# Kernel optimization log

Measured on AMD Instinct MI355X. Metric: run time of the kernel, lower is better.

The kernel has to match this reference:

```python
import jax, jax.numpy as jnp
import numpy as np

N, D_IN, D_H, K, E = 100000, 128, 256, 16, 3200000


def setup_inputs() -> dict:
    key = jax.random.key(0)
    ks = jax.random.split(key, 6)
    x = jax.random.normal(ks[0], (N, D_IN), dtype=jnp.float32)
    edge_index = jax.random.randint(ks[1], (2, E), 0, N, dtype=jnp.int64)
    # Linear params (stored as [in, out] for x @ W + b)
    W1 = jax.random.normal(ks[2], (D_IN, D_H), dtype=jnp.float32) * 0.05
    b1 = jnp.zeros((D_H,), dtype=jnp.float32)
    W2 = jax.random.normal(ks[3], (D_H, K), dtype=jnp.float32) * 0.05
    b2 = jnp.zeros((K,), dtype=jnp.float32)
    return {"x": x, "edge_index": edge_index, "W1": W1, "b1": b1, "W2": W2, "b2": b2}


def reference(x, edge_index, W1, b1, W2, b2):
    # 2-layer MLP + row softmax -> soft cluster assignments C [N, K]
    h = jax.nn.relu(x @ W1 + b1)
    C = jax.nn.softmax(h @ W2 + b2, axis=1)
    # trace((C C^T)^T @ adj) == sum over edges (u,v) of C[u] . C[v]
    # (exact, incl. duplicate edges, since to_dense_adj scatter-adds 1 per edge)
    src, dst = edge_index[0], edge_index[1]
    edge_sum = jnp.sum(C[src] * C[dst])  # [E, K] gathered dot products, reduced
    num_edges = jnp.asarray(edge_index.shape[1], dtype=C.dtype)  # adj.sum()
    modularity_loss = -edge_sum / num_edges
    return (C, modularity_loss)
```

## Files before the change

### kernel.cpp

```cpp
#include <hip/hip_runtime.h>

#define N_NODES 100000
#define D_INF   128
#define D_HID   256
#define K_CL    16
#define N_TILES (N_NODES / 16)
#define N_EDGES 3200000
#define EDGE_BLOCKS (N_EDGES / 1024)

typedef __attribute__((ext_vector_type(8))) __bf16  bf16x8;
typedef __attribute__((ext_vector_type(8))) unsigned short u16x8;
typedef __attribute__((ext_vector_type(4))) float   f32x4;
typedef __attribute__((ext_vector_type(2))) float   f32x2;
typedef __attribute__((ext_vector_type(4))) unsigned int u32x4;

__device__ __forceinline__ unsigned short f2bf(float f) {
    unsigned int u = __builtin_bit_cast(unsigned int, f);
    u += 0x7fffu + ((u >> 16) & 1u);
    return (unsigned short)(u >> 16);
}

__global__ void prep_kernel(const float* __restrict__ W1,
                            const float* __restrict__ W2,
                            unsigned short* __restrict__ w1t,
                            unsigned short* __restrict__ w2t)
{
    const int i = blockIdx.x * 256 + threadIdx.x;
    if (i < D_INF * D_HID) {
        const int n = i >> 7, k = i & 127;
        w1t[i] = f2bf(W1[k * D_HID + n]);
    }
    if (i < D_HID * K_CL) {
        const int t = i >> 8, n = i & 255;
        w2t[i] = f2bf(W2[n * K_CL + t]);
    }
}

#define W1S 136
#define CHS 40

__global__ __launch_bounds__(256, 2) void mlp_kernel(
    const float* __restrict__ x, const unsigned short* __restrict__ W1T,
    const float* __restrict__ b1, const unsigned short* __restrict__ W2T,
    const float* __restrict__ b2, float* __restrict__ C,
    unsigned char* __restrict__ C8)
{
    __shared__ unsigned short w1s[256 * W1S];
    __shared__ unsigned short chbuf[4][2][16 * CHS];
    __shared__ float b1s[D_HID];

    const int tid  = threadIdx.x;
    const int wv   = tid >> 6;
    const int lane = tid & 63;
    const int c    = lane & 15;
    const int q    = lane >> 4;

    #pragma unroll
    for (int it = 0; it < 16; ++it) {
        const int idx = it * 256 + tid;
        const int row = idx >> 4, ch = idx & 15;
        const uint4 v = ((const uint4*)W1T)[idx];
        *(uint4*)&w1s[row * W1S + ch * 8] = v;
    }
    if (tid < D_HID) b1s[tid] = b1[tid];

    bf16x8 w2f[8];
    #pragma unroll
    for (int kc2 = 0; kc2 < 8; ++kc2)
        w2f[kc2] = *(const bf16x8*)(W2T + (size_t)c * D_HID + kc2 * 32 + q * 8);
    const float b2v = b2[c];
    __syncthreads();

    unsigned short* const chA = &chbuf[wv][0][0];
    unsigned short* const chB = &chbuf[wv][1][0];

    const int wid     = blockIdx.x * 4 + wv;
    const int wstride = gridDim.x * 4;

    float4 xraw[8];
    {
        const float* xr = x + (size_t)(wid * 16 + c) * D_INF + q * 8;
        #pragma unroll
        for (int j = 0; j < 8; ++j)
            xraw[j] = *(const float4*)(xr + (j >> 1) * 32 + (j & 1) * 4);
    }

    for (int tile = wid; tile < N_TILES; tile += wstride) {
        const int m0 = tile * 16;

        const int nxt = tile + wstride;
        float4 xnxt[8];
        if (nxt < N_TILES) {
            const float* xr = x + (size_t)(nxt * 16 + c) * D_INF + q * 8;
            #pragma unroll
            for (int j = 0; j < 8; ++j)
                xnxt[j] = *(const float4*)(xr + (j >> 1) * 32 + (j & 1) * 4);
        }

        bf16x8 afr[4];
        #pragma unroll
        for (int kc = 0; kc < 4; ++kc) {
            const float4 xa = xraw[kc * 2], xb = xraw[kc * 2 + 1];
            u16x8 af;
            af[0] = f2bf(xa.x); af[1] = f2bf(xa.y); af[2] = f2bf(xa.z); af[3] = f2bf(xa.w);
            af[4] = f2bf(xb.x); af[5] = f2bf(xb.y); af[6] = f2bf(xb.z); af[7] = f2bf(xb.w);
            afr[kc] = __builtin_bit_cast(bf16x8, af);
        }

        f32x4 acc2 = (f32x4){0.f, 0.f, 0.f, 0.f};
        #pragma unroll
        for (int kc2 = 0; kc2 < 8; ++kc2) {
            unsigned short* const cb = (kc2 & 1) ? chB : chA;
            #pragma unroll
            for (int half = 0; half < 2; ++half) {
                const int nt = kc2 * 2 + half;
                f32x4 a1 = (f32x4){0.f, 0.f, 0.f, 0.f};
                #pragma unroll
                for (int kc = 0; kc < 4; ++kc) {
                    const bf16x8 bf =
                        *(const bf16x8*)&w1s[(nt * 16 + c) * W1S + kc * 32 + q * 8];
                    a1 = __builtin_amdgcn_mfma_f32_16x16x32_bf16(afr[kc], bf, a1, 0, 0, 0);
                }
                const float bv = b1s[nt * 16 + c];
                #pragma unroll
                for (int r = 0; r < 4; ++r)
                    cb[(4 * q + r) * CHS + half * 16 + c] =
                        f2bf(fmaxf(a1[r] + bv, 0.f));
            }
            const bf16x8 a2 = *(const bf16x8*)&cb[c * CHS + q * 8];
            acc2 = __builtin_amdgcn_mfma_f32_16x16x32_bf16(a2, w2f[kc2], acc2, 0, 0, 0);
        }

        #pragma unroll
        for (int r = 0; r < 4; ++r) {
            const float l = acc2[r] + b2v;
            float mx = l;
            mx = fmaxf(mx, __shfl_xor(mx, 1));
            mx = fmaxf(mx, __shfl_xor(mx, 2));
            mx = fmaxf(mx, __shfl_xor(mx, 4));
            mx = fmaxf(mx, __shfl_xor(mx, 8));
            const float e = __expf(l - mx);
            float sm = e;
            sm += __shfl_xor(sm, 1);
            sm += __shfl_xor(sm, 2);
            sm += __shfl_xor(sm, 4);
            sm += __shfl_xor(sm, 8);
            const float p = e / sm;
            const size_t o = (size_t)(m0 + 4 * q + r) * K_CL + c;
            C[o]  = p;
            C8[o] = (unsigned char)
                (__builtin_amdgcn_cvt_pk_fp8_f32(p, p, 0, false) & 0xff);
        }

        if (nxt < N_TILES) {
            #pragma unroll
            for (int j = 0; j < 8; ++j) xraw[j] = xnxt[j];
        }
    }
}

__global__ __launch_bounds__(256, 5) void edge_kernel(
    const int* __restrict__ ei, const unsigned char* __restrict__ C8,
    float* __restrict__ partials)
{
    __shared__ float red[4];
    const int tid  = threadIdx.x;
    const int lane = tid & 63;
    const int wv   = tid >> 6;
    const int base = (blockIdx.x * 4 + wv) * 256;

    int u[4], v[4];
    #pragma unroll
    for (int j = 0; j < 4; ++j) {
        u[j] = ei[base + j * 64 + lane];
        v[j] = ei[N_EDGES + base + j * 64 + lane];
    }

    u32x4 A[4], B[4];
    #pragma unroll
    for (int j = 0; j < 4; ++j) {
        A[j] = *(const u32x4*)(C8 + (size_t)u[j] * 16);
        B[j] = *(const u32x4*)(C8 + (size_t)v[j] * 16);
    }

    float s0 = 0.f, s1 = 0.f, s2 = 0.f, s3 = 0.f;
    #pragma unroll
    for (int j = 0; j < 4; ++j) {
        float t = 0.f;
        #pragma unroll
        for (int d = 0; d < 4; ++d) {
            const f32x2 a0 = __builtin_amdgcn_cvt_pk_f32_fp8(A[j][d], false);
            const f32x2 a1 = __builtin_amdgcn_cvt_pk_f32_fp8(A[j][d], true);
            const f32x2 b0 = __builtin_amdgcn_cvt_pk_f32_fp8(B[j][d], false);
            const f32x2 b1 = __builtin_amdgcn_cvt_pk_f32_fp8(B[j][d], true);
            t = fmaf(a0[0], b0[0], t);
            t = fmaf(a0[1], b0[1], t);
            t = fmaf(a1[0], b1[0], t);
            t = fmaf(a1[1], b1[1], t);
        }
        if (j == 0) s0 = t; else if (j == 1) s1 = t;
        else if (j == 2) s2 = t; else s3 = t;
    }
    float s = (s0 + s1) + (s2 + s3);

    s += __shfl_xor(s, 1);
    s += __shfl_xor(s, 2);
    s += __shfl_xor(s, 4);
    s += __shfl_xor(s, 8);
    s += __shfl_xor(s, 16);
    s += __shfl_xor(s, 32);
    if (lane == 0) red[wv] = s;
    __syncthreads();
    if (tid == 0) partials[blockIdx.x] = red[0] + red[1] + red[2] + red[3];
}

__global__ __launch_bounds__(256) void finalize_kernel(
    const float* __restrict__ partials, float* __restrict__ out)
{
    __shared__ float red[4];
    const int tid = threadIdx.x;
    float s = 0.f;
    for (int i = tid; i < EDGE_BLOCKS; i += 256) s += partials[i];
    s += __shfl_xor(s, 1);
    s += __shfl_xor(s, 2);
    s += __shfl_xor(s, 4);
    s += __shfl_xor(s, 8);
    s += __shfl_xor(s, 16);
    s += __shfl_xor(s, 32);
    if ((tid & 63) == 0) red[tid >> 6] = s;
    __syncthreads();
    if (tid == 0)
        out[(size_t)N_NODES * K_CL] =
            -(red[0] + red[1] + red[2] + red[3]) / (float)N_EDGES;
}

extern "C" void kernel_launch(void* const* d_in, const int* in_sizes, int n_in,
                              void* d_out, int out_size, void* d_ws, size_t ws_size,
                              hipStream_t stream) {
    const float* x  = (const float*)d_in[0];
    const int*   ei = (const int*)  d_in[1];
    const float* W1 = (const float*)d_in[2];
    const float* b1 = (const float*)d_in[3];
    const float* W2 = (const float*)d_in[4];
    const float* b2 = (const float*)d_in[5];
    float* out = (float*)d_out;

    unsigned short* w1t      = (unsigned short*)d_ws;
    unsigned short* w2t      = (unsigned short*)((char*)d_ws + 65536);
    unsigned char*  C8       = (unsigned char*)((char*)d_ws + 73760);
    float*          partials = (float*)((char*)d_ws + 1673760);

    prep_kernel<<<128, 256, 0, stream>>>(W1, W2, w1t, w2t);
    mlp_kernel<<<512, 256, 0, stream>>>(x, w1t, b1, w2t, b2, out, C8);
    edge_kernel<<<EDGE_BLOCKS, 256, 0, stream>>>(ei, C8, partials);
    finalize_kernel<<<1, 256, 0, stream>>>(partials, out);
}
```

Baseline: 152.8 us.

## Fold weight prep into MLP kernel and finalize into edge kernel via ticket

Removes the separate prep kernel: each MLP block now converts and transposes W1 and W2 from fp32 to bf16 itself while loading them into shared memory and registers. Removes the finalize kernel: edge blocks publish their partial sums and take an atomic ticket, and the last block to arrive performs the final reduction. This cuts two kernel launches and their inter-kernel gaps. In exchange, every MLP block does a redundant strided fp32 weight read and conversion, and the edge path adds an atomic and a fence per block.

```diff
diff --git a/kernel.cpp b/kernel.cpp
--- a/kernel.cpp
+++ b/kernel.cpp
@@ -20,30 +20,14 @@
     return (unsigned short)(u >> 16);
 }
 
-__global__ void prep_kernel(const float* __restrict__ W1,
-                            const float* __restrict__ W2,
-                            unsigned short* __restrict__ w1t,
-                            unsigned short* __restrict__ w2t)
-{
-    const int i = blockIdx.x * 256 + threadIdx.x;
-    if (i < D_INF * D_HID) {
-        const int n = i >> 7, k = i & 127;
-        w1t[i] = f2bf(W1[k * D_HID + n]);
-    }
-    if (i < D_HID * K_CL) {
-        const int t = i >> 8, n = i & 255;
-        w2t[i] = f2bf(W2[n * K_CL + t]);
-    }
-}
-
 #define W1S 136
 #define CHS 40
 
 __global__ __launch_bounds__(256, 2) void mlp_kernel(
-    const float* __restrict__ x, const unsigned short* __restrict__ W1T,
-    const float* __restrict__ b1, const unsigned short* __restrict__ W2T,
+    const float* __restrict__ x, const float* __restrict__ W1,
+    const float* __restrict__ b1, const float* __restrict__ W2,
     const float* __restrict__ b2, float* __restrict__ C,
-    unsigned char* __restrict__ C8)
+    unsigned char* __restrict__ C8, unsigned int* __restrict__ ticket)
 {
     __shared__ unsigned short w1s[256 * W1S];
     __shared__ unsigned short chbuf[4][2][16 * CHS];
@@ -55,19 +39,27 @@
     const int c    = lane & 15;
     const int q    = lane >> 4;
 
-    #pragma unroll
-    for (int it = 0; it < 16; ++it) {
-        const int idx = it * 256 + tid;
-        const int row = idx >> 4, ch = idx & 15;
-        const uint4 v = ((const uint4*)W1T)[idx];
-        *(uint4*)&w1s[row * W1S + ch * 8] = v;
+    if (blockIdx.x == 0 && tid == 0)
+        __hip_atomic_store(ticket, 0u, __ATOMIC_RELAXED,
+                           __HIP_MEMORY_SCOPE_AGENT);
+
+    #pragma unroll 4
+    for (int k = 0; k < 128; k += 2) {
+        const unsigned int lo = f2bf(W1[k * D_HID + tid]);
+        const unsigned int hi = f2bf(W1[(k + 1) * D_HID + tid]);
+        *(unsigned int*)&w1s[tid * W1S + k] = lo | (hi << 16);
     }
     if (tid < D_HID) b1s[tid] = b1[tid];
 
     bf16x8 w2f[8];
     #pragma unroll
-    for (int kc2 = 0; kc2 < 8; ++kc2)
-        w2f[kc2] = *(const bf16x8*)(W2T + (size_t)c * D_HID + kc2 * 32 + q * 8);
+    for (int kc2 = 0; kc2 < 8; ++kc2) {
+        u16x8 t;
+        #pragma unroll
+        for (int j = 0; j < 8; ++j)
+            t[j] = f2bf(W2[(kc2 * 32 + q * 8 + j) * K_CL + c]);
+        w2f[kc2] = __builtin_bit_cast(bf16x8, t);
+    }
     const float b2v = b2[c];
     __syncthreads();
 
@@ -161,9 +153,11 @@
 
 __global__ __launch_bounds__(256, 5) void edge_kernel(
     const int* __restrict__ ei, const unsigned char* __restrict__ C8,
-    float* __restrict__ partials)
+    float* __restrict__ partials, unsigned int* __restrict__ ticket,
+    float* __restrict__ out)
 {
     __shared__ float red[4];
+    __shared__ unsigned int is_last;
     const int tid  = threadIdx.x;
     const int lane = tid & 63;
     const int wv   = tid >> 6;
@@ -211,27 +205,33 @@
     s += __shfl_xor(s, 32);
     if (lane == 0) red[wv] = s;
     __syncthreads();
-    if (tid == 0) partials[blockIdx.x] = red[0] + red[1] + red[2] + red[3];
-}
-
-__global__ __launch_bounds__(256) void finalize_kernel(
-    const float* __restrict__ partials, float* __restrict__ out)
-{
-    __shared__ float red[4];
-    const int tid = threadIdx.x;
-    float s = 0.f;
-    for (int i = tid; i < EDGE_BLOCKS; i += 256) s += partials[i];
-    s += __shfl_xor(s, 1);
-    s += __shfl_xor(s, 2);
-    s += __shfl_xor(s, 4);
-    s += __shfl_xor(s, 8);
-    s += __shfl_xor(s, 16);
-    s += __shfl_xor(s, 32);
-    if ((tid & 63) == 0) red[tid >> 6] = s;
+    if (tid == 0) {
+        const float bs = red[0] + red[1] + red[2] + red[3];
+        __hip_atomic_store(&partials[blockIdx.x], bs, __ATOMIC_RELAXED,
+                           __HIP_MEMORY_SCOPE_AGENT);
+        __threadfence();
+        const unsigned int old = atomicAdd(ticket, 1u);
+        is_last = (old == (unsigned int)(EDGE_BLOCKS - 1)) ? 1u : 0u;
+    }
     __syncthreads();
-    if (tid == 0)
-        out[(size_t)N_NODES * K_CL] =
-            -(red[0] + red[1] + red[2] + red[3]) / (float)N_EDGES;
+
+    if (is_last) {
+        float t = 0.f;
+        for (int i = tid; i < EDGE_BLOCKS; i += 256)
+            t += __hip_atomic_load(&partials[i], __ATOMIC_RELAXED,
+                                   __HIP_MEMORY_SCOPE_AGENT);
+        t += __shfl_xor(t, 1);
+        t += __shfl_xor(t, 2);
+        t += __shfl_xor(t, 4);
+        t += __shfl_xor(t, 8);
+        t += __shfl_xor(t, 16);
+        t += __shfl_xor(t, 32);
+        if (lane == 0) red[wv] = t;
+        __syncthreads();
+        if (tid == 0)
+            out[(size_t)N_NODES * K_CL] =
+                -(red[0] + red[1] + red[2] + red[3]) / (float)N_EDGES;
+    }
 }
 
 extern "C" void kernel_launch(void* const* d_in, const int* in_sizes, int n_in,
@@ -245,13 +245,10 @@
     const float* b2 = (const float*)d_in[5];
     float* out = (float*)d_out;
 
-    unsigned short* w1t      = (unsigned short*)d_ws;
-    unsigned short* w2t      = (unsigned short*)((char*)d_ws + 65536);
-    unsigned char*  C8       = (unsigned char*)((char*)d_ws + 73760);
-    float*          partials = (float*)((char*)d_ws + 1673760);
-
-    prep_kernel<<<128, 256, 0, stream>>>(W1, W2, w1t, w2t);
-    mlp_kernel<<<512, 256, 0, stream>>>(x, w1t, b1, w2t, b2, out, C8);
-    edge_kernel<<<EDGE_BLOCKS, 256, 0, stream>>>(ei, C8, partials);
-    finalize_kernel<<<1, 256, 0, stream>>>(partials, out);
-}
+    unsigned char* C8       = (unsigned char*)d_ws;
+    float*         partials = (float*)((char*)d_ws + 1600000);
+    unsigned int*  ticket   = (unsigned int*)((char*)d_ws + 1612500);
+
+    mlp_kernel<<<512, 256, 0, stream>>>(x, W1, b1, W2, b2, out, C8, ticket);
+    edge_kernel<<<EDGE_BLOCKS, 256, 0, stream>>>(ei, C8, partials, ticket, out);
+}
```

Result: slower. 227.2 us (+48.7%).

## Process two row tiles per wave and fold weight conversion into MLP kernel

Applied to the files above, without the earlier changes.

Removes the separate weight-prep kernel; each MLP block now converts and transposes W1/W2 from fp32 into bf16 LDS/registers directly. Each wave handles two 16-row tiles per iteration, reusing each W1 LDS fragment for two MFMAs and giving independent MFMA chains, with the next pair's x prefetched. This saves a launch and LDS reads per tile but adds redundant strided fp32 weight loads in every block and more register pressure.

```diff
diff --git a/kernel.cpp b/kernel.cpp
--- a/kernel.cpp
+++ b/kernel.cpp
@@ -4,7 +4,7 @@
 #define D_INF   128
 #define D_HID   256
 #define K_CL    16
-#define N_TILES (N_NODES / 16)
+#define N_PAIRS (N_NODES / 32)
 #define N_EDGES 3200000
 #define EDGE_BLOCKS (N_EDGES / 1024)
 
@@ -20,28 +20,12 @@
     return (unsigned short)(u >> 16);
 }
 
-__global__ void prep_kernel(const float* __restrict__ W1,
-                            const float* __restrict__ W2,
-                            unsigned short* __restrict__ w1t,
-                            unsigned short* __restrict__ w2t)
-{
-    const int i = blockIdx.x * 256 + threadIdx.x;
-    if (i < D_INF * D_HID) {
-        const int n = i >> 7, k = i & 127;
-        w1t[i] = f2bf(W1[k * D_HID + n]);
-    }
-    if (i < D_HID * K_CL) {
-        const int t = i >> 8, n = i & 255;
-        w2t[i] = f2bf(W2[n * K_CL + t]);
-    }
-}
-
 #define W1S 136
 #define CHS 40
 
 __global__ __launch_bounds__(256, 2) void mlp_kernel(
-    const float* __restrict__ x, const unsigned short* __restrict__ W1T,
-    const float* __restrict__ b1, const unsigned short* __restrict__ W2T,
+    const float* __restrict__ x, const float* __restrict__ W1,
+    const float* __restrict__ b1, const float* __restrict__ W2,
     const float* __restrict__ b2, float* __restrict__ C,
     unsigned char* __restrict__ C8)
 {
@@ -55,19 +39,23 @@
     const int c    = lane & 15;
     const int q    = lane >> 4;
 
-    #pragma unroll
-    for (int it = 0; it < 16; ++it) {
-        const int idx = it * 256 + tid;
-        const int row = idx >> 4, ch = idx & 15;
-        const uint4 v = ((const uint4*)W1T)[idx];
-        *(uint4*)&w1s[row * W1S + ch * 8] = v;
+    #pragma unroll 4
+    for (int k = 0; k < 128; k += 2) {
+        const unsigned int lo = f2bf(W1[k * D_HID + tid]);
+        const unsigned int hi = f2bf(W1[(k + 1) * D_HID + tid]);
+        *(unsigned int*)&w1s[tid * W1S + k] = lo | (hi << 16);
     }
     if (tid < D_HID) b1s[tid] = b1[tid];
 
     bf16x8 w2f[8];
     #pragma unroll
-    for (int kc2 = 0; kc2 < 8; ++kc2)
-        w2f[kc2] = *(const bf16x8*)(W2T + (size_t)c * D_HID + kc2 * 32 + q * 8);
+    for (int kc2 = 0; kc2 < 8; ++kc2) {
+        u16x8 t;
+        #pragma unroll
+        for (int j = 0; j < 8; ++j)
+            t[j] = f2bf(W2[(kc2 * 32 + q * 8 + j) * K_CL + c]);
+        w2f[kc2] = __builtin_bit_cast(bf16x8, t);
+    }
     const float b2v = b2[c];
     __syncthreads();
 
@@ -77,84 +65,100 @@
     const int wid     = blockIdx.x * 4 + wv;
     const int wstride = gridDim.x * 4;
 
-    float4 xraw[8];
+    float4 xraw[16];
     {
-        const float* xr = x + (size_t)(wid * 16 + c) * D_INF + q * 8;
-        #pragma unroll
-        for (int j = 0; j < 8; ++j)
-            xraw[j] = *(const float4*)(xr + (j >> 1) * 32 + (j & 1) * 4);
-    }
-
-    for (int tile = wid; tile < N_TILES; tile += wstride) {
-        const int m0 = tile * 16;
-
-        const int nxt = tile + wstride;
-        float4 xnxt[8];
-        if (nxt < N_TILES) {
-            const float* xr = x + (size_t)(nxt * 16 + c) * D_INF + q * 8;
-            #pragma unroll
-            for (int j = 0; j < 8; ++j)
-                xnxt[j] = *(const float4*)(xr + (j >> 1) * 32 + (j & 1) * 4);
-        }
-
-        bf16x8 afr[4];
+        const float* xr0 = x + (size_t)(wid * 32 + c)      * D_INF + q * 8;
+        const float* xr1 = x + (size_t)(wid * 32 + 16 + c) * D_INF + q * 8;
+        #pragma unroll
+        for (int j = 0; j < 8; ++j) {
+            xraw[j]     = *(const float4*)(xr0 + (j >> 1) * 32 + (j & 1) * 4);
+            xraw[8 + j] = *(const float4*)(xr1 + (j >> 1) * 32 + (j & 1) * 4);
+        }
+    }
+
+    for (int pair = wid; pair < N_PAIRS; pair += wstride) {
+        const int m0 = pair * 32;
+
+        bf16x8 afr0[4], afr1[4];
         #pragma unroll
         for (int kc = 0; kc < 4; ++kc) {
-            const float4 xa = xraw[kc * 2], xb = xraw[kc * 2 + 1];
-            u16x8 af;
+            const float4 xa = xraw[kc * 2],     xb = xraw[kc * 2 + 1];
+            const float4 ya = xraw[8 + kc * 2], yb = xraw[8 + kc * 2 + 1];
+            u16x8 af, ag;
             af[0] = f2bf(xa.x); af[1] = f2bf(xa.y); af[2] = f2bf(xa.z); af[3] = f2bf(xa.w);
             af[4] = f2bf(xb.x); af[5] = f2bf(xb.y); af[6] = f2bf(xb.z); af[7] = f2bf(xb.w);
-            afr[kc] = __builtin_bit_cast(bf16x8, af);
-        }
-
-        f32x4 acc2 = (f32x4){0.f, 0.f, 0.f, 0.f};
+            ag[0] = f2bf(ya.x); ag[1] = f2bf(ya.y); ag[2] = f2bf(ya.z); ag[3] = f2bf(ya.w);
+            ag[4] = f2bf(yb.x); ag[5] = f2bf(yb.y); ag[6] = f2bf(yb.z); ag[7] = f2bf(yb.w);
+            afr0[kc] = __builtin_bit_cast(bf16x8, af);
+            afr1[kc] = __builtin_bit_cast(bf16x8, ag);
+        }
+
+        const int nxt = pair + wstride;
+        if (nxt < N_PAIRS) {
+            const float* xr0 = x + (size_t)(nxt * 32 + c)      * D_INF + q * 8;
+            const float* xr1 = x + (size_t)(nxt * 32 + 16 + c) * D_INF + q * 8;
+            #pragma unroll
+            for (int j = 0; j < 8; ++j) {
+                xraw[j]     = *(const float4*)(xr0 + (j >> 1) * 32 + (j & 1) * 4);
+                xraw[8 + j] = *(const float4*)(xr1 + (j >> 1) * 32 + (j & 1) * 4);
+            }
+        }
+
+        f32x4 acc2a = (f32x4){0.f, 0.f, 0.f, 0.f};
+        f32x4 acc2b = (f32x4){0.f, 0.f, 0.f, 0.f};
         #pragma unroll
         for (int kc2 = 0; kc2 < 8; ++kc2) {
-            unsigned short* const cb = (kc2 & 1) ? chB : chA;
             #pragma unroll
             for (int half = 0; half < 2; ++half) {
                 const int nt = kc2 * 2 + half;
-                f32x4 a1 = (f32x4){0.f, 0.f, 0.f, 0.f};
+                f32x4 a1a = (f32x4){0.f, 0.f, 0.f, 0.f};
+                f32x4 a1b = (f32x4){0.f, 0.f, 0.f, 0.f};
                 #pragma unroll
                 for (int kc = 0; kc < 4; ++kc) {
                     const bf16x8 bf =
                         *(const bf16x8*)&w1s[(nt * 16 + c) * W1S + kc * 32 + q * 8];
-                    a1 = __builtin_amdgcn_mfma_f32_16x16x32_bf16(afr[kc], bf, a1, 0, 0, 0);
+                    a1a = __builtin_amdgcn_mfma_f32_16x16x32_bf16(afr0[kc], bf, a1a, 0, 0, 0);
+                    a1b = __builtin_amdgcn_mfma_f32_16x16x32_bf16(afr1[kc], bf, a1b, 0, 0, 0);
                 }
                 const float bv = b1s[nt * 16 + c];
                 #pragma unroll
-                for (int r = 0; r < 4; ++r)
-                    cb[(4 * q + r) * CHS + half * 16 + c] =
-                        f2bf(fmaxf(a1[r] + bv, 0.f));
+                for (int r = 0; r < 4; ++r) {
+                    chA[(4 * q + r) * CHS + half * 16 + c] =
+                        f2bf(fmaxf(a1a[r] + bv, 0.f));
+                    chB[(4 * q + r) * CHS + half * 16 + c] =
+                        f2bf(fmaxf(a1b[r] + bv, 0.f));
+                }
             }
-            const bf16x8 a2 = *(const bf16x8*)&cb[c * CHS + q * 8];
-            acc2 = __builtin_amdgcn_mfma_f32_16x16x32_bf16(a2, w2f[kc2], acc2, 0, 0, 0);
-        }
-
-        #pragma unroll
-        for (int r = 0; r < 4; ++r) {
-            const float l = acc2[r] + b2v;
-            float mx = l;
-            mx = fmaxf(mx, __shfl_xor(mx, 1));
-            mx = fmaxf(mx, __shfl_xor(mx, 2));
-            mx = fmaxf(mx, __shfl_xor(mx, 4));
-            mx = fmaxf(mx, __shfl_xor(mx, 8));
-            const float e = __expf(l - mx);
-            float sm = e;
-            sm += __shfl_xor(sm, 1);
-            sm += __shfl_xor(sm, 2);
-            sm += __shfl_xor(sm, 4);
-            sm += __shfl_xor(sm, 8);
-            const float p = e / sm;
-            const size_t o = (size_t)(m0 + 4 * q + r) * K_CL + c;
-            C[o]  = p;
-            C8[o] = (unsigned char)
-                (__builtin_amdgcn_cvt_pk_fp8_f32(p, p, 0, false) & 0xff);
-        }
-
-        if (nxt < N_TILES) {
+            const bf16x8 a2a = *(const bf16x8*)&chA[c * CHS + q * 8];
+            const bf16x8 a2b = *(const bf16x8*)&chB[c * CHS + q * 8];
+            acc2a = __builtin_amdgcn_mfma_f32_16x16x32_bf16(a2a, w2f[kc2], acc2a, 0, 0, 0);
+            acc2b = __builtin_amdgcn_mfma_f32_16x16x32_bf16(a2b, w2f[kc2], acc2b, 0, 0, 0);
+        }
+
+        #pragma unroll
+        for (int t2 = 0; t2 < 2; ++t2) {
+            const f32x4 acc2 = t2 ? acc2b : acc2a;
+            const int mb = m0 + t2 * 16;
             #pragma unroll
-            for (int j = 0; j < 8; ++j) xraw[j] = xnxt[j];
+            for (int r = 0; r < 4; ++r) {
+                const float l = acc2[r] + b2v;
+                float mx = l;
+                mx = fmaxf(mx, __shfl_xor(mx, 1));
+                mx = fmaxf(mx, __shfl_xor(mx, 2));
+                mx = fmaxf(mx, __shfl_xor(mx, 4));
+                mx = fmaxf(mx, __shfl_xor(mx, 8));
+                const float e = __expf(l - mx);
+                float sm = e;
+                sm += __shfl_xor(sm, 1);
+                sm += __shfl_xor(sm, 2);
+                sm += __shfl_xor(sm, 4);
+                sm += __shfl_xor(sm, 8);
+                const float p = e / sm;
+                const size_t o = (size_t)(mb + 4 * q + r) * K_CL + c;
+                C[o]  = p;
+                C8[o] = (unsigned char)
+                    (__builtin_amdgcn_cvt_pk_fp8_f32(p, p, 0, false) & 0xff);
+            }
         }
     }
 }
@@ -245,13 +249,10 @@
     const float* b2 = (const float*)d_in[5];
     float* out = (float*)d_out;
 
-    unsigned short* w1t      = (unsigned short*)d_ws;
-    unsigned short* w2t      = (unsigned short*)((char*)d_ws + 65536);
-    unsigned char*  C8       = (unsigned char*)((char*)d_ws + 73760);
-    float*          partials = (float*)((char*)d_ws + 1673760);
-
-    prep_kernel<<<128, 256, 0, stream>>>(W1, W2, w1t, w2t);
-    mlp_kernel<<<512, 256, 0, stream>>>(x, w1t, b1, w2t, b2, out, C8);
+    unsigned char* C8       = (unsigned char*)d_ws;
+    float*         partials = (float*)((char*)d_ws + 1600000);
+
+    mlp_kernel<<<512, 256, 0, stream>>>(x, W1, b1, W2, b2, out, C8);
     edge_kernel<<<EDGE_BLOCKS, 256, 0, stream>>>(ei, C8, partials);
     finalize_kernel<<<1, 256, 0, stream>>>(partials, out);
 }
```

Result: slower. 158.4 us (+3.6%).
